# Performance work log

Hardware: AMD Instinct MI355X
Metric: run time of the kernel (lower is better)

## Reference

```python
import jax, jax.numpy as jnp
import numpy as np

B, L, N = 16, 512, 32          # batch, seq_length, feature_size
E = 128                        # embed_size == frequency_size (number_frequency=1)
EMB = 8                        # embedding_dim
FCH = 64                       # fc_hidden_dim
H = 256                        # hidden_size
PRE = 96                       # pre_length
LAMBDA = 0.01                  # sparsity_threshold
SCALE = 0.02                   # init_scale


def softshrink(v, lambd=LAMBDA):
    return jnp.where(v > lambd, v - lambd, jnp.where(v < -lambd, v + lambd, 0.0))


def setup_inputs() -> dict:
    key = jax.random.key(0)
    ks = jax.random.split(key, 16)
    f32 = jnp.float32
    return {
        "x": jax.random.normal(ks[0], (B, L, N), f32),
        "emb": jax.random.normal(ks[1], (1, E), f32),
        "w0": SCALE * jax.random.normal(ks[2], (2, E, E), f32),
        "b0": SCALE * jax.random.normal(ks[3], (2, E), f32),
        "w1": SCALE * jax.random.normal(ks[4], (2, E, E), f32),
        "b1": SCALE * jax.random.normal(ks[5], (2, E), f32),
        "w2": SCALE * jax.random.normal(ks[6], (2, E, E), f32),
        "b2": SCALE * jax.random.normal(ks[7], (2, E), f32),
        "emb10": jax.random.normal(ks[8], (L, EMB), f32),
        "fc1_w": jax.random.normal(ks[9], (FCH, E * EMB), f32) / np.sqrt(E * EMB),
        "fc1_b": jnp.zeros((FCH,), f32),
        "fc2_w": jax.random.normal(ks[10], (H, FCH), f32) / np.sqrt(FCH),
        "fc2_b": jnp.zeros((H,), f32),
        "fc3_w": jax.random.normal(ks[11], (PRE, H), f32) / np.sqrt(H),
        "fc3_b": jnp.zeros((PRE,), f32),
    }


def _diag(w):
    # einsum 'bli,ii->bli' multiplies by the DIAGONAL of w only
    return jnp.diagonal(w, axis1=-2, axis2=-1)


def reference(x, emb, w0, b0, w1, b1, w2, b2, emb10,
              fc1_w, fc1_b, fc2_w, fc2_b, fc3_w, fc3_b):
    Bb = x.shape[0]
    xt = jnp.transpose(x, (0, 2, 1)).reshape(Bb, -1)          # [B, N*L]
    tok = xt[:, :, None] * emb                                 # [B, N*L, E]
    xf = jnp.fft.rfft(tok, axis=1, norm="ortho")               # [B, N*L//2+1, E] complex
    bias = xf

    # --- fourierGC (faithful to the torch op ordering, incl. o_real reuse) ---
    relu = jax.nn.relu
    d00, d01 = _diag(w0[0]), _diag(w0[1])
    o_r = relu(xf.real * d00 - xf.imag * d01 + b0[0])
    o_i = relu(xf.imag * d00 + xf.real * d01 + b0[1])
    prev = softshrink(jnp.stack([o_r, o_i], axis=-1))

    # middle layer (num_layers=3 -> one): note o_i uses the UPDATED o_r, as in torch
    d10, d11 = _diag(w1[0]), _diag(w1[1])
    o_r_new = relu(o_r * d10 - o_i * d11 + b1[0])
    o_i = relu(o_i * d10 + o_r_new * d11 + b1[1])
    o_r = o_r_new
    prev = softshrink(jnp.stack([o_r, o_i], axis=-1)) + prev

    # last layer
    d20, d21 = _diag(w2[0]), _diag(w2[1])
    o_r_new = relu(o_r * d20 - o_i * d21 + b2[0])
    o_i = relu(o_i * d20 + o_r_new * d21 + b2[1])
    z = softshrink(jnp.stack([o_r_new, o_i], axis=-1)) + prev
    zc = jax.lax.complex(z[..., 0], z[..., 1])

    xf = zc + bias
    xt = jnp.fft.irfft(xf, n=N * L, axis=1, norm="ortho")      # [B, N*L, E]
    xt = xt.reshape(Bb, N, L, E)
    xt = jnp.transpose(xt, (0, 1, 3, 2))                        # [B, N, E, L]
    h = jnp.matmul(xt, emb10)                                   # [B, N, E, EMB]
    h = h.reshape(Bb, N, E * EMB)

    lrelu = lambda v: jax.nn.leaky_relu(v, 0.01)
    h = lrelu(h @ fc1_w.T + fc1_b)
    h = lrelu(h @ fc2_w.T + fc2_b)
    out = h @ fc3_w.T + fc3_b                                   # [B, N, PRE]
    return out[:, 0, :]                                         # target_idx = 0
```

## Files before the change

kernel.cpp:

```cpp
#include <hip/hip_runtime.h>
#include <math.h>

#define Bsz   16
#define Lseq  512
#define Nfeat 32
#define E     128
#define EMB   8
#define FCH   64
#define Hd    256
#define PRE   96
#define M     16384
#define MH    8193
#define LAMBDA 0.01f

#define OFF_W   0
#define OFF_G   32768
#define OFF_CS  32768
#define OFF_X   557056
#define XSTRIDE 8200
#define OFF_P   819456

__global__ void k_twiddle(float* __restrict__ ws) {
  int k = blockIdx.x * 256 + threadIdx.x;
  float s, c;
  sincosf((float)k * 3.83495196971410293e-4f, &s, &c);
  ws[OFF_W + 2 * k]     = c;
  ws[OFF_W + 2 * k + 1] = s;
}

__global__ void k_fft1(const float* __restrict__ x, float* __restrict__ ws) {
  int b = blockIdx.y;
  int t1base = blockIdx.x * 2;
  __shared__ float xcol[2][128];
  int tid = threadIdx.x;
  int t1loc = tid >> 7, idx = tid & 127;
  {
    int t = (t1base + t1loc) + 128 * idx;
    int n = t >> 9, l = t & 511;
    xcol[t1loc][idx] = x[b * (Lseq * Nfeat) + l * Nfeat + n];
  }
  __syncthreads();
  int f1 = idx, t1 = t1base + t1loc;
  float c1 = ws[OFF_W + 2 * (f1 << 7)];
  float s1 = ws[OFF_W + 2 * (f1 << 7) + 1];
  float c2 = c1 * c1 - s1 * s1;
  float s2 = 2.0f * s1 * c1;
  float cA = 1.f, sA = 0.f, cB = c1, sB = s1;
  float grA = 0.f, giA = 0.f, grB = 0.f, giB = 0.f;
  #pragma unroll 8
  for (int t2 = 0; t2 < 128; t2 += 2) {
    float xv0 = xcol[t1loc][t2];
    float xv1 = xcol[t1loc][t2 + 1];
    grA = fmaf(xv0, cA, grA);  giA = fmaf(xv0, -sA, giA);
    grB = fmaf(xv1, cB, grB);  giB = fmaf(xv1, -sB, giB);
    float cn = cA * c2 - sA * s2; sA = sA * c2 + cA * s2; cA = cn;
    cn = cB * c2 - sB * s2;       sB = sB * c2 + cB * s2; cB = cn;
  }
  float gr = grA + grB, gi = giA + giB;
  int kk = f1 * t1;
  float cb = ws[OFF_W + 2 * kk], sb = ws[OFF_W + 2 * kk + 1];
  float grr = gr * cb + gi * sb;
  float gii = gi * cb - gr * sb;
  float* G = ws + OFF_G + (((b * 128 + f1) * 128) + t1) * 2;
  G[0] = grr;
  G[1] = gii;
}

__global__ void k_fft2(float* __restrict__ ws) {
  int b = blockIdx.y;
  int f1base = blockIdx.x * 2;
  __shared__ __align__(16) float2 Gs[2][128];
  int tid = threadIdx.x;
  {
    int f1loc = tid >> 7, r = tid & 127;
    Gs[f1loc][r] = ((const float2*)(ws + OFF_G))[(b * 128 + f1base + f1loc) * 128 + r];
  }
  __syncthreads();
  int f2 = tid & 127, f1loc = tid >> 7;
  int f = (f1base + f1loc) + 128 * f2;
  if (f > 8192) return;
  float c1 = ws[OFF_W + 2 * (f2 << 7)];
  float s1 = ws[OFF_W + 2 * (f2 << 7) + 1];
  float c2 = c1 * c1 - s1 * s1;
  float s2 = 2.0f * s1 * c1;
  float cA = 1.f, sA = 0.f, cB = c1, sB = s1;
  float xrA = 0.f, xiA = 0.f, xrB = 0.f, xiB = 0.f;
  #pragma unroll 8
  for (int t1 = 0; t1 < 128; t1 += 2) {
    float2 g0 = Gs[f1loc][t1];
    float2 g1 = Gs[f1loc][t1 + 1];
    xrA = fmaf(g0.x, cA, xrA); xrA = fmaf(g0.y, sA, xrA);
    xiA = fmaf(g0.y, cA, xiA); xiA = fmaf(-g0.x, sA, xiA);
    xrB = fmaf(g1.x, cB, xrB); xrB = fmaf(g1.y, sB, xrB);
    xiB = fmaf(g1.y, cB, xiB); xiB = fmaf(-g1.x, sB, xiB);
    float cn = cA * c2 - sA * s2; sA = sA * c2 + cA * s2; cA = cn;
    cn = cB * c2 - sB * s2;       sB = sB * c2 + cB * s2; cB = cn;
  }
  float* X = ws + OFF_X + (b * XSTRIDE + f) * 2;
  X[0] = xrA + xrB;
  X[1] = xiA + xiB;
}

__global__ void k_cs(const float* __restrict__ emb10, float* __restrict__ ws) {
  __shared__ float e10[Lseq * EMB];
  int tid = threadIdx.x;
  for (int i = tid; i < Lseq * EMB; i += 256) e10[i] = emb10[i];
  __syncthreads();
  int floc = tid >> 5, tl = tid & 31;
  int f = blockIdx.x * 8 + floc;
  if (f > 8192) return;
  const float* wt = ws + OFF_W;
  float ca[EMB], sa[EMB];
  #pragma unroll
  for (int m = 0; m < EMB; ++m) { ca[m] = 0.f; sa[m] = 0.f; }
  #pragma unroll 4
  for (int i = 0; i < 16; ++i) {
    int t = tl + 32 * i;
    int k = (f * t) & (M - 1);
    float cc = wt[2 * k], ss = wt[2 * k + 1];
    const float* er = e10 + t * EMB;
    #pragma unroll
    for (int m = 0; m < EMB; ++m) {
      ca[m] = fmaf(cc, er[m], ca[m]);
      sa[m] = fmaf(ss, er[m], sa[m]);
    }
  }
  #pragma unroll
  for (int off = 16; off >= 1; off >>= 1) {
    #pragma unroll
    for (int m = 0; m < EMB; ++m) {
      ca[m] += __shfl_xor(ca[m], off, 64);
      sa[m] += __shfl_xor(sa[m], off, 64);
    }
  }
  if (tl == 0) {
    float wf = (f == 0 || f == 8192) ? (1.0f / 128.0f) : (2.0f / 128.0f);
    float* o = ws + OFF_CS + f * 16;
    #pragma unroll
    for (int m = 0; m < EMB; ++m) { o[m] = ca[m] * wf; o[8 + m] = sa[m] * wf; }
  }
}

#define FCHUNK 128
__global__ void k_gc(const float* __restrict__ emb,
                     const float* __restrict__ w0, const float* __restrict__ b0,
                     const float* __restrict__ w1, const float* __restrict__ b1,
                     const float* __restrict__ w2, const float* __restrict__ b2,
                     float* __restrict__ ws) {
  int b = blockIdx.y;
  int fstart = blockIdx.x * FCHUNK;
  int fcount = min(FCHUNK, MH - fstart);
  __shared__ __align__(16) float Xs[FCHUNK * 2];
  __shared__ __align__(16) float CSs[FCHUNK * 16];
  __shared__ float red[E * EMB];
  int tid = threadIdx.x;
  {
    const float4* src = (const float4*)(ws + OFF_X + (b * XSTRIDE + fstart) * 2);
    float4* dst = (float4*)Xs;
    for (int j = tid; j < (fcount * 2 + 3) / 4; j += 256) dst[j] = src[j];
    const float4* src2 = (const float4*)(ws + OFF_CS + fstart * 16);
    float4* dst2 = (float4*)CSs;
    for (int j = tid; j < fcount * 4; j += 256) dst2[j] = src2[j];
  }
  __syncthreads();
  int e = tid & 127, fh = tid >> 7;
  float se  = emb[e] * (1.0f / 128.0f);
  float d00 = w0[e * 129], d01 = w0[E * E + e * 129];
  float c00 = b0[e],       c01 = b0[E + e];
  float d10 = w1[e * 129], d11 = w1[E * E + e * 129];
  float c10 = b1[e],       c11 = b1[E + e];
  float d20 = w2[e * 129], d21 = w2[E * E + e * 129];
  float c20 = b2[e],       c21 = b2[E + e];
  float acc[EMB];
  #pragma unroll
  for (int m = 0; m < EMB; ++m) acc[m] = 0.f;

  for (int i = fh; i < fcount; i += 2) {
    float xr = Xs[2 * i] * se, xi = Xs[2 * i + 1] * se;
    float or0 = fmaxf(fmaf(xr, d00, fmaf(-xi, d01, c00)), 0.f);
    float oi0 = fmaxf(fmaf(xi, d00, fmaf(xr, d01, c01)), 0.f);
    float pr = fmaxf(or0 - LAMBDA, 0.f), pi = fmaxf(oi0 - LAMBDA, 0.f);
    float or1 = fmaxf(fmaf(or0, d10, fmaf(-oi0, d11, c10)), 0.f);
    float oi1 = fmaxf(fmaf(oi0, d10, fmaf(or1, d11, c11)), 0.f);
    pr += fmaxf(or1 - LAMBDA, 0.f); pi += fmaxf(oi1 - LAMBDA, 0.f);
    float or2 = fmaxf(fmaf(or1, d20, fmaf(-oi1, d21, c20)), 0.f);
    float oi2 = fmaxf(fmaf(oi1, d20, fmaf(or2, d21, c21)), 0.f);
    float zr = fmaxf(or2 - LAMBDA, 0.f) + pr;
    float zi = fmaxf(oi2 - LAMBDA, 0.f) + pi;
    const float4* cs4 = (const float4*)&CSs[i * 16];
    float4 cA = cs4[0], cB = cs4[1], sA = cs4[2], sB = cs4[3];
    acc[0] = fmaf(zr, cA.x, fmaf(-zi, sA.x, acc[0]));
    acc[1] = fmaf(zr, cA.y, fmaf(-zi, sA.y, acc[1]));
    acc[2] = fmaf(zr, cA.z, fmaf(-zi, sA.z, acc[2]));
    acc[3] = fmaf(zr, cA.w, fmaf(-zi, sA.w, acc[3]));
    acc[4] = fmaf(zr, cB.x, fmaf(-zi, sB.x, acc[4]));
    acc[5] = fmaf(zr, cB.y, fmaf(-zi, sB.y, acc[5]));
    acc[6] = fmaf(zr, cB.z, fmaf(-zi, sB.z, acc[6]));
    acc[7] = fmaf(zr, cB.w, fmaf(-zi, sB.w, acc[7]));
  }
  if (fh == 1) {
    #pragma unroll
    for (int m = 0; m < EMB; ++m) red[e * EMB + m] = acc[m];
  }
  __syncthreads();
  if (fh == 0) {
    float* P = ws + OFF_P + (blockIdx.x * 16 + b) * (E * EMB) + e * EMB;
    #pragma unroll
    for (int m = 0; m < EMB; ++m) P[m] = acc[m] + red[e * EMB + m];
  }
}

__global__ void k_fc(const float* __restrict__ x, const float* __restrict__ emb,
                     const float* __restrict__ emb10,
                     const float* __restrict__ fc1w, const float* __restrict__ fc1b,
                     const float* __restrict__ fc2w, const float* __restrict__ fc2b,
                     const float* __restrict__ fc3w, const float* __restrict__ fc3b,
                     const float* __restrict__ ws, float* __restrict__ out) {
  int b = blockIdx.x;
  __shared__ float h0s[E * EMB];
  __shared__ float h1s[FCH];
  __shared__ float h2s[Hd];
  __shared__ float hxs[EMB];
  __shared__ float scratch[256];
  int tid = threadIdx.x;
  {
    int m = tid & 7, g = tid >> 3;
    float p = 0.f;
    for (int l = g; l < Lseq; l += 32)
      p = fmaf(x[b * (Lseq * Nfeat) + l * Nfeat], emb10[l * EMB + m], p);
    scratch[tid] = p;
  }
  __syncthreads();
  if (tid < 8) {
    float s = 0.f;
    for (int g = 0; g < 32; ++g) s += scratch[g * 8 + tid];
    hxs[tid] = s;
  }
  __syncthreads();
  for (int k = tid; k < E * EMB; k += 256) {
    float a = emb[k >> 3] * hxs[k & 7];
    const float* P = ws + OFF_P + b * (E * EMB) + k;
    #pragma unroll 13
    for (int c = 0; c < 65; ++c) a += P[c * (16 * E * EMB)];
    h0s[k] = a;
  }
  __syncthreads();
  {
    int o = tid & 63, kc = tid >> 6;
    const float* wrow = fc1w + o * (E * EMB) + kc * 256;
    const float* hh = h0s + kc * 256;
    float a = 0.f;
    #pragma unroll 8
    for (int k = 0; k < 256; ++k) a = fmaf(hh[k], wrow[k], a);
    scratch[tid] = a;
  }
  __syncthreads();
  if (tid < FCH) {
    float a = fc1b[tid] + scratch[tid] + scratch[tid + 64] +
              scratch[tid + 128] + scratch[tid + 192];
    h1s[tid] = a > 0.f ? a : 0.01f * a;
  }
  __syncthreads();
  {
    float a = fc2b[tid];
    const float* wrow = fc2w + tid * FCH;
    #pragma unroll 8
    for (int c = 0; c < FCH; ++c) a = fmaf(h1s[c], wrow[c], a);
    h2s[tid] = a > 0.f ? a : 0.01f * a;
  }
  __syncthreads();
  {
    int o = tid & 127, kc = tid >> 7;
    float a = 0.f;
    if (o < PRE) {
      const float* wrow = fc3w + o * Hd + kc * 128;
      const float* hh = h2s + kc * 128;
      #pragma unroll 8
      for (int k = 0; k < 128; ++k) a = fmaf(hh[k], wrow[k], a);
    }
    scratch[tid] = a;
  }
  __syncthreads();
  if (tid < PRE) out[b * PRE + tid] = fc3b[tid] + scratch[tid] + scratch[tid + 128];
}

extern "C" void kernel_launch(void* const* d_in, const int* in_sizes, int n_in,
                              void* d_out, int out_size, void* d_ws, size_t ws_size,
                              hipStream_t stream) {
  const float* x     = (const float*)d_in[0];
  const float* emb   = (const float*)d_in[1];
  const float* w0    = (const float*)d_in[2];
  const float* b0    = (const float*)d_in[3];
  const float* w1    = (const float*)d_in[4];
  const float* b1    = (const float*)d_in[5];
  const float* w2    = (const float*)d_in[6];
  const float* b2    = (const float*)d_in[7];
  const float* emb10 = (const float*)d_in[8];
  const float* fc1w  = (const float*)d_in[9];
  const float* fc1b  = (const float*)d_in[10];
  const float* fc2w  = (const float*)d_in[11];
  const float* fc2b  = (const float*)d_in[12];
  const float* fc3w  = (const float*)d_in[13];
  const float* fc3b  = (const float*)d_in[14];
  float* ws  = (float*)d_ws;
  float* out = (float*)d_out;

  k_twiddle<<<dim3(64), 256, 0, stream>>>(ws);
  k_fft1<<<dim3(64, Bsz), 256, 0, stream>>>(x, ws);
  k_fft2<<<dim3(64, Bsz), 256, 0, stream>>>(ws);
  k_cs<<<dim3(1025), 256, 0, stream>>>(emb10, ws);
  k_gc<<<dim3(65, Bsz), 256, 0, stream>>>(emb, w0, b0, w1, b1, w2, b2, ws);
  k_fc<<<dim3(Bsz), 256, 0, stream>>>(x, emb, emb10, fc1w, fc1b, fc2w, fc2b,
                                      fc3w, fc3b, ws, out);
}
```

Baseline: 181.6 us.

## Fuse FFT stages and graph-conv into fewer kernels, compute twiddles inline

Removes the twiddle table kernel and computes sin/cos on the fly. The first FFT stage and the cos/sin projection table now run as two independent branches of a single k_prep launch. The second FFT stage is fused into the graph-conv kernel, which now works per f1 column, so the X spectrum never round-trips through global memory. This cuts the launch count from six to three and drops intermediate traffic. In exchange it costs extra sincosf work, and the final FC reduction now sums 128 partial slices per element instead of 65.

Result: faster. 176.6 us (-2.7%).

```diff
diff --git a/kernel.cpp b/kernel.cpp
--- a/kernel.cpp
+++ b/kernel.cpp
@@ -13,154 +13,134 @@
 #define MH    8193
 #define LAMBDA 0.01f
 
-#define OFF_W   0
-#define OFF_G   32768
-#define OFF_CS  32768
-#define OFF_X   557056
-#define XSTRIDE 8200
-#define OFF_P   819456
-
-__global__ void k_twiddle(float* __restrict__ ws) {
-  int k = blockIdx.x * 256 + threadIdx.x;
-  float s, c;
-  sincosf((float)k * 3.83495196971410293e-4f, &s, &c);
-  ws[OFF_W + 2 * k]     = c;
-  ws[OFF_W + 2 * k + 1] = s;
-}
-
-__global__ void k_fft1(const float* __restrict__ x, float* __restrict__ ws) {
-  int b = blockIdx.y;
-  int t1base = blockIdx.x * 2;
-  __shared__ float xcol[2][128];
-  int tid = threadIdx.x;
-  int t1loc = tid >> 7, idx = tid & 127;
-  {
-    int t = (t1base + t1loc) + 128 * idx;
-    int n = t >> 9, l = t & 511;
-    xcol[t1loc][idx] = x[b * (Lseq * Nfeat) + l * Nfeat + n];
-  }
-  __syncthreads();
-  int f1 = idx, t1 = t1base + t1loc;
-  float c1 = ws[OFF_W + 2 * (f1 << 7)];
-  float s1 = ws[OFF_W + 2 * (f1 << 7) + 1];
-  float c2 = c1 * c1 - s1 * s1;
-  float s2 = 2.0f * s1 * c1;
-  float cA = 1.f, sA = 0.f, cB = c1, sB = s1;
-  float grA = 0.f, giA = 0.f, grB = 0.f, giB = 0.f;
-  #pragma unroll 8
-  for (int t2 = 0; t2 < 128; t2 += 2) {
-    float xv0 = xcol[t1loc][t2];
-    float xv1 = xcol[t1loc][t2 + 1];
-    grA = fmaf(xv0, cA, grA);  giA = fmaf(xv0, -sA, giA);
-    grB = fmaf(xv1, cB, grB);  giB = fmaf(xv1, -sB, giB);
-    float cn = cA * c2 - sA * s2; sA = sA * c2 + cA * s2; cA = cn;
-    cn = cB * c2 - sB * s2;       sB = sB * c2 + cB * s2; cB = cn;
-  }
-  float gr = grA + grB, gi = giA + giB;
-  int kk = f1 * t1;
-  float cb = ws[OFF_W + 2 * kk], sb = ws[OFF_W + 2 * kk + 1];
-  float grr = gr * cb + gi * sb;
-  float gii = gi * cb - gr * sb;
-  float* G = ws + OFF_G + (((b * 128 + f1) * 128) + t1) * 2;
-  G[0] = grr;
-  G[1] = gii;
-}
-
-__global__ void k_fft2(float* __restrict__ ws) {
-  int b = blockIdx.y;
-  int f1base = blockIdx.x * 2;
-  __shared__ __align__(16) float2 Gs[2][128];
-  int tid = threadIdx.x;
-  {
-    int f1loc = tid >> 7, r = tid & 127;
-    Gs[f1loc][r] = ((const float2*)(ws + OFF_G))[(b * 128 + f1base + f1loc) * 128 + r];
-  }
-  __syncthreads();
-  int f2 = tid & 127, f1loc = tid >> 7;
-  int f = (f1base + f1loc) + 128 * f2;
-  if (f > 8192) return;
-  float c1 = ws[OFF_W + 2 * (f2 << 7)];
-  float s1 = ws[OFF_W + 2 * (f2 << 7) + 1];
-  float c2 = c1 * c1 - s1 * s1;
-  float s2 = 2.0f * s1 * c1;
-  float cA = 1.f, sA = 0.f, cB = c1, sB = s1;
-  float xrA = 0.f, xiA = 0.f, xrB = 0.f, xiB = 0.f;
-  #pragma unroll 8
-  for (int t1 = 0; t1 < 128; t1 += 2) {
-    float2 g0 = Gs[f1loc][t1];
-    float2 g1 = Gs[f1loc][t1 + 1];
-    xrA = fmaf(g0.x, cA, xrA); xrA = fmaf(g0.y, sA, xrA);
-    xiA = fmaf(g0.y, cA, xiA); xiA = fmaf(-g0.x, sA, xiA);
-    xrB = fmaf(g1.x, cB, xrB); xrB = fmaf(g1.y, sB, xrB);
-    xiB = fmaf(g1.y, cB, xiB); xiB = fmaf(-g1.x, sB, xiB);
-    float cn = cA * c2 - sA * s2; sA = sA * c2 + cA * s2; cA = cn;
-    cn = cB * c2 - sB * s2;       sB = sB * c2 + cB * s2; cB = cn;
-  }
-  float* X = ws + OFF_X + (b * XSTRIDE + f) * 2;
-  X[0] = xrA + xrB;
-  X[1] = xiA + xiB;
-}
-
-__global__ void k_cs(const float* __restrict__ emb10, float* __restrict__ ws) {
-  __shared__ float e10[Lseq * EMB];
-  int tid = threadIdx.x;
-  for (int i = tid; i < Lseq * EMB; i += 256) e10[i] = emb10[i];
-  __syncthreads();
-  int floc = tid >> 5, tl = tid & 31;
-  int f = blockIdx.x * 8 + floc;
-  if (f > 8192) return;
-  const float* wt = ws + OFF_W;
-  float ca[EMB], sa[EMB];
-  #pragma unroll
-  for (int m = 0; m < EMB; ++m) { ca[m] = 0.f; sa[m] = 0.f; }
-  #pragma unroll 4
-  for (int i = 0; i < 16; ++i) {
-    int t = tl + 32 * i;
-    int k = (f * t) & (M - 1);
-    float cc = wt[2 * k], ss = wt[2 * k + 1];
-    const float* er = e10 + t * EMB;
-    #pragma unroll
-    for (int m = 0; m < EMB; ++m) {
-      ca[m] = fmaf(cc, er[m], ca[m]);
-      sa[m] = fmaf(ss, er[m], sa[m]);
-    }
-  }
-  #pragma unroll
-  for (int off = 16; off >= 1; off >>= 1) {
-    #pragma unroll
-    for (int m = 0; m < EMB; ++m) {
-      ca[m] += __shfl_xor(ca[m], off, 64);
-      sa[m] += __shfl_xor(sa[m], off, 64);
-    }
-  }
-  if (tl == 0) {
-    float wf = (f == 0 || f == 8192) ? (1.0f / 128.0f) : (2.0f / 128.0f);
-    float* o = ws + OFF_CS + f * 16;
-    #pragma unroll
-    for (int m = 0; m < EMB; ++m) { o[m] = ca[m] * wf; o[8 + m] = sa[m] * wf; }
-  }
-}
-
-#define FCHUNK 128
-__global__ void k_gc(const float* __restrict__ emb,
-                     const float* __restrict__ w0, const float* __restrict__ b0,
-                     const float* __restrict__ w1, const float* __restrict__ b1,
-                     const float* __restrict__ w2, const float* __restrict__ b2,
-                     float* __restrict__ ws) {
-  int b = blockIdx.y;
-  int fstart = blockIdx.x * FCHUNK;
-  int fcount = min(FCHUNK, MH - fstart);
-  __shared__ __align__(16) float Xs[FCHUNK * 2];
-  __shared__ __align__(16) float CSs[FCHUNK * 16];
-  __shared__ float red[E * EMB];
-  int tid = threadIdx.x;
-  {
-    const float4* src = (const float4*)(ws + OFF_X + (b * XSTRIDE + fstart) * 2);
-    float4* dst = (float4*)Xs;
-    for (int j = tid; j < (fcount * 2 + 3) / 4; j += 256) dst[j] = src[j];
-    const float4* src2 = (const float4*)(ws + OFF_CS + fstart * 16);
-    float4* dst2 = (float4*)CSs;
-    for (int j = tid; j < fcount * 4; j += 256) dst2[j] = src2[j];
+#define OFF_G   0
+#define OFF_CS  524288
+#define OFF_P   655376
+
+#define TWO_PI_M   3.83495196971410293e-4f
+#define TWO_PI_128 4.90873852123405245e-2f
+
+__global__ __launch_bounds__(256)
+void k_prep(const float* __restrict__ x, const float* __restrict__ emb10,
+            float* __restrict__ ws) {
+  __shared__ float smem[Lseq * EMB];
+  int bid = blockIdx.x, tid = threadIdx.x;
+  if (bid < 1025) {
+    for (int i = tid; i < Lseq * EMB; i += 256) smem[i] = emb10[i];
+    __syncthreads();
+    int floc = tid >> 5, tl = tid & 31;
+    int f = bid * 8 + floc;
+    if (f > 8192) return;
+    float ca[EMB], sa[EMB];
+    #pragma unroll
+    for (int m = 0; m < EMB; ++m) { ca[m] = 0.f; sa[m] = 0.f; }
+    #pragma unroll 4
+    for (int i = 0; i < 16; ++i) {
+      int t = tl + 32 * i;
+      int k = (f * t) & (M - 1);
+      float ss, cc;
+      sincosf((float)k * TWO_PI_M, &ss, &cc);
+      const float* er = smem + t * EMB;
+      #pragma unroll
+      for (int m = 0; m < EMB; ++m) {
+        ca[m] = fmaf(cc, er[m], ca[m]);
+        sa[m] = fmaf(ss, er[m], sa[m]);
+      }
+    }
+    #pragma unroll
+    for (int off = 16; off >= 1; off >>= 1) {
+      #pragma unroll
+      for (int m = 0; m < EMB; ++m) {
+        ca[m] += __shfl_xor(ca[m], off, 64);
+        sa[m] += __shfl_xor(sa[m], off, 64);
+      }
+    }
+    if (tl == 0) {
+      float wf = (f == 0 || f == 8192) ? (1.0f / 128.0f) : (2.0f / 128.0f);
+      float* o = ws + OFF_CS + f * 16;
+      #pragma unroll
+      for (int m = 0; m < EMB; ++m) { o[m] = ca[m] * wf; o[8 + m] = sa[m] * wf; }
+    }
+  } else {
+    int v = bid - 1025;
+    int b = v >> 6, t1base = (v & 63) << 1;
+    int t1loc = tid >> 7, idx = tid & 127;
+    {
+      int t = (t1base + t1loc) + 128 * idx;
+      int n = t >> 9, l = t & 511;
+      smem[t1loc * 128 + idx] = x[b * (Lseq * Nfeat) + l * Nfeat + n];
+    }
+    __syncthreads();
+    int f1 = idx, t1 = t1base + t1loc;
+    float s1, c1; sincosf((float)f1 * TWO_PI_128, &s1, &c1);
+    float c2 = c1 * c1 - s1 * s1, s2 = 2.f * s1 * c1;
+    float cA = 1.f, sA = 0.f, cB = c1, sB = s1;
+    float grA = 0.f, giA = 0.f, grB = 0.f, giB = 0.f;
+    const float* xc = smem + t1loc * 128;
+    #pragma unroll 8
+    for (int t2 = 0; t2 < 128; t2 += 2) {
+      float x0 = xc[t2], x1 = xc[t2 + 1];
+      grA = fmaf(x0, cA, grA); giA = fmaf(x0, -sA, giA);
+      grB = fmaf(x1, cB, grB); giB = fmaf(x1, -sB, giB);
+      float cn = cA * c2 - sA * s2; sA = sA * c2 + cA * s2; cA = cn;
+      cn = cB * c2 - sB * s2;       sB = sB * c2 + cB * s2; cB = cn;
+    }
+    float gr = grA + grB, gi = giA + giB;
+    float sb, cb; sincosf((float)(f1 * t1) * TWO_PI_M, &sb, &cb);
+    float grr = gr * cb + gi * sb;
+    float gii = gi * cb - gr * sb;
+    float* G = ws + OFF_G + ((b * 128 + f1) * 128 + t1) * 2;
+    G[0] = grr;
+    G[1] = gii;
+  }
+}
+
+__global__ __launch_bounds__(256)
+void k_gcf(const float* __restrict__ emb,
+           const float* __restrict__ w0, const float* __restrict__ b0,
+           const float* __restrict__ w1, const float* __restrict__ b1,
+           const float* __restrict__ w2, const float* __restrict__ b2,
+           float* __restrict__ ws) {
+  int f1 = blockIdx.x, b = blockIdx.y, tid = threadIdx.x;
+  int nf2 = (f1 == 0) ? 65 : 64;
+  __shared__ float2 Gs[128];
+  __shared__ float Xp[4][65][2];
+  __shared__ float CSs[65 * 16];
+  {
+    const float2* gsrc = (const float2*)(ws + OFF_G + (b * 128 + f1) * 256);
+    if (tid < 128) Gs[tid] = gsrc[tid];
+    for (int j = tid; j < nf2 * 16; j += 256) {
+      int i = j >> 4, m = j & 15;
+      CSs[j] = ws[OFF_CS + (f1 + 128 * i) * 16 + m];
+    }
+  }
+  __syncthreads();
+  {
+    int f2 = tid & 63, q = tid >> 6;
+    int r = (f2 * q) & 3;
+    float c = (r == 0) ? 1.f : (r == 2) ? -1.f : 0.f;
+    float s = (r == 1) ? 1.f : (r == 3) ? -1.f : 0.f;
+    float s1, c1; sincosf((float)f2 * TWO_PI_128, &s1, &c1);
+    float xr = 0.f, xi = 0.f;
+    int t1 = q * 32;
+    #pragma unroll 8
+    for (int k = 0; k < 32; ++k) {
+      float2 g = Gs[t1 + k];
+      xr = fmaf(g.x, c, xr); xr = fmaf(g.y, s, xr);
+      xi = fmaf(g.y, c, xi); xi = fmaf(-g.x, s, xi);
+      float cn = c * c1 - s * s1; s = s * c1 + c * s1; c = cn;
+    }
+    Xp[q][f2][0] = xr; Xp[q][f2][1] = xi;
+    if (f1 == 0 && f2 == 0) {
+      float er = 0.f, ei = 0.f;
+      #pragma unroll 8
+      for (int k = 0; k < 32; ++k) {
+        float2 g = Gs[t1 + k];
+        float sg = ((t1 + k) & 1) ? -1.f : 1.f;
+        er = fmaf(g.x, sg, er); ei = fmaf(g.y, sg, ei);
+      }
+      Xp[q][64][0] = er; Xp[q][64][1] = ei;
+    }
   }
   __syncthreads();
   int e = tid & 127, fh = tid >> 7;
@@ -175,8 +155,9 @@
   #pragma unroll
   for (int m = 0; m < EMB; ++m) acc[m] = 0.f;
 
-  for (int i = fh; i < fcount; i += 2) {
-    float xr = Xs[2 * i] * se, xi = Xs[2 * i + 1] * se;
+  for (int i = fh; i < nf2; i += 2) {
+    float xr = ((Xp[0][i][0] + Xp[1][i][0]) + (Xp[2][i][0] + Xp[3][i][0])) * se;
+    float xi = ((Xp[0][i][1] + Xp[1][i][1]) + (Xp[2][i][1] + Xp[3][i][1])) * se;
     float or0 = fmaxf(fmaf(xr, d00, fmaf(-xi, d01, c00)), 0.f);
     float oi0 = fmaxf(fmaf(xi, d00, fmaf(xr, d01, c01)), 0.f);
     float pr = fmaxf(or0 - LAMBDA, 0.f), pi = fmaxf(oi0 - LAMBDA, 0.f);
@@ -187,35 +168,32 @@
     float oi2 = fmaxf(fmaf(oi1, d20, fmaf(or2, d21, c21)), 0.f);
     float zr = fmaxf(or2 - LAMBDA, 0.f) + pr;
     float zi = fmaxf(oi2 - LAMBDA, 0.f) + pi;
-    const float4* cs4 = (const float4*)&CSs[i * 16];
-    float4 cA = cs4[0], cB = cs4[1], sA = cs4[2], sB = cs4[3];
-    acc[0] = fmaf(zr, cA.x, fmaf(-zi, sA.x, acc[0]));
-    acc[1] = fmaf(zr, cA.y, fmaf(-zi, sA.y, acc[1]));
-    acc[2] = fmaf(zr, cA.z, fmaf(-zi, sA.z, acc[2]));
-    acc[3] = fmaf(zr, cA.w, fmaf(-zi, sA.w, acc[3]));
-    acc[4] = fmaf(zr, cB.x, fmaf(-zi, sB.x, acc[4]));
-    acc[5] = fmaf(zr, cB.y, fmaf(-zi, sB.y, acc[5]));
-    acc[6] = fmaf(zr, cB.z, fmaf(-zi, sB.z, acc[6]));
-    acc[7] = fmaf(zr, cB.w, fmaf(-zi, sB.w, acc[7]));
-  }
+    const float* cs = &CSs[i * 16];
+    #pragma unroll
+    for (int m = 0; m < EMB; ++m)
+      acc[m] = fmaf(zr, cs[m], fmaf(-zi, cs[8 + m], acc[m]));
+  }
+  __syncthreads();
+  float* red = CSs;
   if (fh == 1) {
     #pragma unroll
     for (int m = 0; m < EMB; ++m) red[e * EMB + m] = acc[m];
   }
   __syncthreads();
   if (fh == 0) {
-    float* P = ws + OFF_P + (blockIdx.x * 16 + b) * (E * EMB) + e * EMB;
+    float* P = ws + OFF_P + (f1 * 16 + b) * (E * EMB) + e * EMB;
     #pragma unroll
     for (int m = 0; m < EMB; ++m) P[m] = acc[m] + red[e * EMB + m];
   }
 }
 
-__global__ void k_fc(const float* __restrict__ x, const float* __restrict__ emb,
-                     const float* __restrict__ emb10,
-                     const float* __restrict__ fc1w, const float* __restrict__ fc1b,
-                     const float* __restrict__ fc2w, const float* __restrict__ fc2b,
-                     const float* __restrict__ fc3w, const float* __restrict__ fc3b,
-                     const float* __restrict__ ws, float* __restrict__ out) {
+__global__ __launch_bounds__(256)
+void k_fc(const float* __restrict__ x, const float* __restrict__ emb,
+          const float* __restrict__ emb10,
+          const float* __restrict__ fc1w, const float* __restrict__ fc1b,
+          const float* __restrict__ fc2w, const float* __restrict__ fc2b,
+          const float* __restrict__ fc3w, const float* __restrict__ fc3b,
+          const float* __restrict__ ws, float* __restrict__ out) {
   int b = blockIdx.x;
   __shared__ float h0s[E * EMB];
   __shared__ float h1s[FCH];
@@ -240,8 +218,8 @@
   for (int k = tid; k < E * EMB; k += 256) {
     float a = emb[k >> 3] * hxs[k & 7];
     const float* P = ws + OFF_P + b * (E * EMB) + k;
-    #pragma unroll 13
-    for (int c = 0; c < 65; ++c) a += P[c * (16 * E * EMB)];
+    #pragma unroll 16
+    for (int c = 0; c < 128; ++c) a += P[c * (16 * E * EMB)];
     h0s[k] = a;
   }
   __syncthreads();
@@ -305,11 +283,8 @@
   float* ws  = (float*)d_ws;
   float* out = (float*)d_out;
 
-  k_twiddle<<<dim3(64), 256, 0, stream>>>(ws);
-  k_fft1<<<dim3(64, Bsz), 256, 0, stream>>>(x, ws);
-  k_fft2<<<dim3(64, Bsz), 256, 0, stream>>>(ws);
-  k_cs<<<dim3(1025), 256, 0, stream>>>(emb10, ws);
-  k_gc<<<dim3(65, Bsz), 256, 0, stream>>>(emb, w0, b0, w1, b1, w2, b2, ws);
+  k_prep<<<dim3(2049), 256, 0, stream>>>(x, emb10, ws);
+  k_gcf<<<dim3(128, Bsz), 256, 0, stream>>>(emb, w0, b0, w1, b1, w2, b2, ws);
   k_fc<<<dim3(Bsz), 256, 0, stream>>>(x, emb, emb10, fc1w, fc1b, fc2w, fc2b,
                                       fc3w, fc3b, ws, out);
 }
```
